# Performance work log

Measured on AMD Instinct MI355X. Metric: run time of the kernel, lower is better.

Reference implementation:

```python
import jax, jax.numpy as jnp
import numpy as np

# Correlation hyperparameters (from init_kwargs):
PAD = 4            # pad_size
KERNEL = 1         # kernel_size (point-wise)
MD = 4             # max_displacement
STRIDE1 = 1
STRIDE2 = 1

B, C, H, W = 8, 256, 96, 160


def setup_inputs() -> dict:
    key = jax.random.key(0)
    k1, k2 = jax.random.split(key)
    input1 = jax.random.normal(k1, (B, C, H, W), dtype=jnp.float32)
    input2 = jax.random.normal(k2, (B, C, H, W), dtype=jnp.float32)
    return {"input1": input1, "input2": input2}


def reference(input1, input2):
    """FlowNet-style correlation cost volume.

    out[b, (dy+MD)*D + (dx+MD), y, x] = (1/C) * sum_c in1[b,c,y,x] * in2pad[b,c,y+dy+PAD, x+dx+PAD]
    where in2pad is input2 zero-padded by PAD and D = 2*MD+1. With PAD == MD,
    kernel_size == 1, stride1 == stride2 == 1 the output is [B, D*D, H, W].
    """
    b, c, h, w = input1.shape
    in2p = jnp.pad(input2, ((0, 0), (0, 0), (PAD, PAD), (PAD, PAD)))
    D = 2 * MD + 1
    outs = []
    # Fixed small 81-iteration loop over displacements (not a data dim).
    for dy in range(0, 2 * MD + 1, STRIDE2):
        for dx in range(0, 2 * MD + 1, STRIDE2):
            shifted = jax.lax.dynamic_slice(in2p, (0, 0, dy, dx), (b, c, h, w))
            # mean over channels == sum / (kernel^2 * C) with kernel == 1
            outs.append(jnp.mean(input1 * shifted, axis=1))
    return jnp.stack(outs, axis=1)  # [B, 81, H, W]
```

## Files before the change

### kernel.cpp

```cpp
#include <hip/hip_runtime.h>
#include <stdint.h>

#define B_ 8
#define C_ 256
#define H_ 96
#define W_ 160
#define ND 9
#define NDISP 81
#define NCHUNK 128
#define TX 4
#define NXG 20
#define NTHR 256
#define NCOMP 180
#define IN2_OFF 320
#define ROW_B 352
#define BUF_B 3584
#define NBUF 4
#define NSEG 218
#define HW (H_ * W_)
#define CHSTEP (2 * HW)

typedef __attribute__((ext_vector_type(2))) _Float16 half2v;

__device__ __forceinline__ unsigned pk(float lo, float hi) {
    return __builtin_bit_cast(unsigned, __builtin_amdgcn_cvt_pkrtz(lo, hi));
}
__device__ __forceinline__ float dot2acc(unsigned a, unsigned w, float acc) {
#if __has_builtin(__builtin_amdgcn_fdot2)
    return __builtin_amdgcn_fdot2(__builtin_bit_cast(half2v, a),
                                  __builtin_bit_cast(half2v, w), acc, false);
#else
    half2v av = __builtin_bit_cast(half2v, a);
    half2v wv = __builtin_bit_cast(half2v, w);
    return acc + (float)av.x * (float)wv.x + (float)av.y * (float)wv.y;
#endif
}

__device__ __forceinline__ void block_barrier_lgkm() {
    asm volatile("s_waitcnt lgkmcnt(0)" ::: "memory");
    __builtin_amdgcn_s_barrier();
    asm volatile("" ::: "memory");
    __builtin_amdgcn_sched_barrier(0);
}

__device__ __forceinline__ const float* seg_src(int s, int b, int y, int h,
        const float* in1, const float* in2, int* woff)
{
    if (s < 20) {
        *woff = s * 16;
        return in1 + ((size_t)(b * C_) * H_ + y) * W_ + 80 * h + 4 * s;
    }
    const int t = s - 20;
    const int r = t / 22, k = t - r * 22;
    *woff = IN2_OFF + r * ROW_B + k * 16;
    int row = y + r - 4;
    row = row < 0 ? 0 : (row >= H_ ? H_ - 1 : row);
    int x = 80 * h - 4 + 4 * k;
    x = x < 0 ? 0 : (x > W_ - 4 ? W_ - 4 : x);
    return in2 + ((size_t)(b * C_) * H_ + row) * W_ + x;
}

__global__ __launch_bounds__(NTHR) void corr_rb_kernel(
    const float* __restrict__ in1,
    const float* __restrict__ in2,
    float* __restrict__ out)
{
    __shared__ __align__(16) unsigned lds[NBUF * BUF_B / 4];

    const int tid = threadIdx.x;
    const int b   = blockIdx.x & 7;
    const int idx = blockIdx.x >> 3;
    const int y   = idx >> 1;
    const int h   = idx & 1;

    int w0off = 0;
    const bool v0 = tid < NSEG;
    const float* p0 = in1;
    if (v0) p0 = seg_src(tid, b, y, h, in1, in2, &w0off);

    const bool isComp = (tid < NCOMP);
    const int  dy = isComp ? (tid / NXG) : 0;
    const int  xg = isComp ? (tid % NXG) : 0;
    const int  x0 = 80 * h + TX * xg;
    const bool rowOk = (y + dy - 4 >= 0) && (y + dy - 4 < H_);
    const bool mzW0 = (h == 0) && (xg == 0);
    const bool mzW2 = (h == 1) && (xg == NXG - 1);

    const int aof = 16 * xg;
    const int wof = IN2_OFF + dy * ROW_B + 16 * xg;

    float acc[ND][TX];
    #pragma unroll
    for (int dx = 0; dx < ND; ++dx)
        #pragma unroll
        for (int j = 0; j < TX; ++j) acc[dx][j] = 0.f;

    float4 SAp0, SAp1;
    float4 SBp0, SBp1;

    #define LOADS(S) do {                                                     \
        S##p0 = *(const float4*)(p0);  S##p1 = *(const float4*)(p0 + HW);     \
        p0 += CHSTEP;                                                         \
    } while (0);

    #define CVTW(BUFI, S) do {                                                \
        if (v0) {                                                             \
            char* base = (char*)lds + (BUFI) * BUF_B;                         \
            *(uint4*)(base + w0off) = make_uint4(                             \
                pk(S##p0.x, S##p1.x), pk(S##p0.y, S##p1.y),                   \
                pk(S##p0.z, S##p1.z), pk(S##p0.w, S##p1.w));                  \
        }                                                                     \
    } while (0);

    #define COMPUTE(BUFI)                                                     \
    if (isComp) {                                                             \
        const char* bb = (const char*)lds + (BUFI) * BUF_B;                   \
        uint4 A0 = *(const uint4*)(bb + aof);                                 \
        uint4 W0 = *(const uint4*)(bb + wof);                                 \
        uint4 W1 = *(const uint4*)(bb + wof + 16);                            \
        uint4 W2 = *(const uint4*)(bb + wof + 32);                            \
        if (mzW0) W0 = make_uint4(0u, 0u, 0u, 0u);                            \
        if (mzW2) W2 = make_uint4(0u, 0u, 0u, 0u);                            \
        unsigned a[4]  = {A0.x, A0.y, A0.z, A0.w};                            \
        unsigned w[12] = {W0.x, W0.y, W0.z, W0.w, W1.x, W1.y, W1.z, W1.w,     \
                          W2.x, W2.y, W2.z, W2.w};                            \
        _Pragma("unroll")                                                     \
        for (int dx = 0; dx < ND; ++dx) {                                     \
            _Pragma("unroll")                                                 \
            for (int j = 0; j < TX; ++j)                                      \
                acc[dx][j] = dot2acc(a[j], w[dx + j], acc[dx][j]);            \
        }                                                                     \
    }

    #define BODY(KM4, SWR, SLD, DOW, DOL)                                     \
        if (DOW) { CVTW(((KM4) + 2) & 3, SWR) }                               \
        if (DOL) { LOADS(SLD) }                                               \
        COMPUTE(KM4)                                                          \
        block_barrier_lgkm();

    LOADS(SA)
    CVTW(0, SA)
    LOADS(SA)
    CVTW(1, SA)
    LOADS(SB)
    block_barrier_lgkm();

    #pragma unroll 1
    for (int g = 0; g < 31; ++g) {
        BODY(0, SB, SA, true, true)
        BODY(1, SA, SB, true, true)
        BODY(2, SB, SA, true, true)
        BODY(3, SA, SB, true, true)
    }
    BODY(0, SB, SA, true, true)
    BODY(1, SA, SB, true, false)
    BODY(2, SA, SA, false, false)
    BODY(3, SA, SA, false, false)

    #undef BODY
    #undef COMPUTE
    #undef CVTW
    #undef LOADS

    if (isComp) {
        const float m = rowOk ? (1.0f / (float)C_) : 0.f;
        float* outp = out + ((size_t)(b * NDISP + dy * ND) * H_ + y) * W_ + x0;
        #pragma unroll
        for (int dx = 0; dx < ND; ++dx) {
            float4 o = make_float4(acc[dx][0] * m, acc[dx][1] * m,
                                   acc[dx][2] * m, acc[dx][3] * m);
            *(float4*)(outp + dx * HW) = o;
        }
    }
}

extern "C" void kernel_launch(void* const* d_in, const int* in_sizes, int n_in,
                              void* d_out, int out_size, void* d_ws, size_t ws_size,
                              hipStream_t stream) {
    const float* in1 = (const float*)d_in[0];
    const float* in2 = (const float*)d_in[1];
    float* out = (float*)d_out;

    const int grid = B_ * H_ * 2;
    corr_rb_kernel<<<grid, NTHR, 0, stream>>>(in1, in2, out);
}
```

Before: 113.0 us.

## Deepen global-load prefetch to three register stages and compute before staging

Result: slower. 116.1 us (+2.8%).

```diff
diff --git a/kernel.cpp b/kernel.cpp
--- a/kernel.cpp
+++ b/kernel.cpp
@@ -60,7 +60,7 @@
     return in2 + ((size_t)(b * C_) * H_ + row) * W_ + x;
 }
 
-__global__ __launch_bounds__(NTHR) void corr_rb_kernel(
+__global__ __launch_bounds__(NTHR) void corr_s3_kernel(
     const float* __restrict__ in1,
     const float* __restrict__ in2,
     float* __restrict__ out)
@@ -97,6 +97,7 @@
 
     float4 SAp0, SAp1;
     float4 SBp0, SBp1;
+    float4 SCp0, SCp1;
 
     #define LOADS(S) do {                                                     \
         S##p0 = *(const float4*)(p0);  S##p1 = *(const float4*)(p0 + HW);     \
@@ -132,30 +133,43 @@
         }                                                                     \
     }
 
-    #define BODY(KM4, SWR, SLD, DOW, DOL)                                     \
-        if (DOW) { CVTW(((KM4) + 2) & 3, SWR) }                               \
-        if (DOL) { LOADS(SLD) }                                               \
-        COMPUTE(KM4)                                                          \
+    #define BODY(BUFC, BUFW, SW, SL, DOW, DOL)                                \
+        COMPUTE(BUFC)                                                         \
+        if (DOW) { CVTW(BUFW, SW) }                                           \
+        if (DOL) { LOADS(SL) }                                                \
         block_barrier_lgkm();
 
     LOADS(SA)
     CVTW(0, SA)
+    LOADS(SB)
+    CVTW(1, SB)
+    LOADS(SC)
     LOADS(SA)
-    CVTW(1, SA)
-    LOADS(SB)
     block_barrier_lgkm();
 
     #pragma unroll 1
-    for (int g = 0; g < 31; ++g) {
-        BODY(0, SB, SA, true, true)
-        BODY(1, SA, SB, true, true)
-        BODY(2, SB, SA, true, true)
-        BODY(3, SA, SB, true, true)
-    }
-    BODY(0, SB, SA, true, true)
-    BODY(1, SA, SB, true, false)
-    BODY(2, SA, SA, false, false)
-    BODY(3, SA, SA, false, false)
+    for (int g = 0; g < 10; ++g) {
+        BODY(0, 2, SC, SB, true, true)
+        BODY(1, 3, SA, SC, true, true)
+        BODY(2, 0, SB, SA, true, true)
+        BODY(3, 1, SC, SB, true, true)
+        BODY(0, 2, SA, SC, true, true)
+        BODY(1, 3, SB, SA, true, true)
+        BODY(2, 0, SC, SB, true, true)
+        BODY(3, 1, SA, SC, true, true)
+        BODY(0, 2, SB, SA, true, true)
+        BODY(1, 3, SC, SB, true, true)
+        BODY(2, 0, SA, SC, true, true)
+        BODY(3, 1, SB, SA, true, true)
+    }
+    BODY(0, 2, SC, SB, true, true)
+    BODY(1, 3, SA, SC, true, true)
+    BODY(2, 0, SB, SA, true, true)
+    BODY(3, 1, SC, SB, true, true)
+    BODY(0, 2, SA, SA, true, false)
+    BODY(1, 3, SB, SA, true, false)
+    BODY(2, 0, SA, SA, false, false)
+    COMPUTE(3)
 
     #undef BODY
     #undef COMPUTE
@@ -182,5 +196,5 @@
     float* out = (float*)d_out;
 
     const int grid = B_ * H_ * 2;
-    corr_rb_kernel<<<grid, NTHR, 0, stream>>>(in1, in2, out);
-}
+    corr_s3_kernel<<<grid, NTHR, 0, stream>>>(in1, in2, out);
+}
```
